# Performance work log

Hardware: AMD Instinct MI355X
Metric: run time of the kernel (lower is better)

## Reference

```python
import jax, jax.numpy as jnp
import numpy as np

N_NODES = 100000
N_EDGES = 1600000
F_IN, F_HID, F_OUT = 128, 128, 16
NEG_SLOPE = 0.2


def _glorot(key, shape):
    fan = sum(shape)
    return jax.random.uniform(key, shape, jnp.float32, -1.0, 1.0) * jnp.sqrt(6.0 / fan)


def setup_inputs() -> dict:
    key = jax.random.key(0)
    ks = jax.random.split(key, 16)
    x = jax.random.normal(ks[0], (N_NODES, F_IN), jnp.float32)
    edge_index = jax.random.randint(ks[1], (2, N_EDGES), 0, N_NODES, jnp.int64)
    d1, d2, d3 = F_HID, F_HID // 2, F_OUT
    return {
        'x': x,
        'edge_index': edge_index,
        'W1': _glorot(ks[2], (F_IN, d1)), 'a_src1': _glorot(ks[3], (d1,)), 'a_dst1': _glorot(ks[4], (d1,)), 'b1': jnp.zeros((d1,), jnp.float32),
        'W2': _glorot(ks[5], (d1, d2)), 'a_src2': _glorot(ks[6], (d2,)), 'a_dst2': _glorot(ks[7], (d2,)), 'b2': jnp.zeros((d2,), jnp.float32),
        'W3': _glorot(ks[8], (d2, d3)), 'a_src3': _glorot(ks[9], (d3,)), 'a_dst3': _glorot(ks[10], (d3,)), 'b3': jnp.zeros((d3,), jnp.float32),
    }


def gat_conv(x, src, dst, W, a_s, a_d, b):
    # x: [N, Fin] -> h: [N, Fout]; src/dst: [E] (self-loops included)
    h = x @ W
    e = jax.nn.leaky_relu(h @ a_s, NEG_SLOPE * 0 + NEG_SLOPE)  # placeholder avoided below
    # attention logits per edge: leaky_relu(alpha_src[src] + alpha_dst[dst])
    al_s = h @ a_s  # [N]
    al_d = h @ a_d  # [N]
    logits = jax.nn.leaky_relu(al_s[src] + al_d[dst], NEG_SLOPE)  # [E]
    # numerically stable softmax over incoming edges of each dst node
    m = jax.ops.segment_max(logits, dst, num_segments=N_NODES)
    m = jnp.where(jnp.isfinite(m), m, 0.0)
    ex = jnp.exp(logits - m[dst])
    denom = jax.ops.segment_sum(ex, dst, num_segments=N_NODES)
    alpha = ex / denom[dst]  # self-loops guarantee denom > 0
    out = jax.ops.segment_sum(alpha[:, None] * h[src], dst, num_segments=N_NODES)
    return out + b


def reference(x, edge_index, W1, a_src1, a_dst1, b1, W2, a_src2, a_dst2, b2, W3, a_src3, a_dst3, b3):
    loops = jnp.arange(N_NODES, dtype=edge_index.dtype)
    src = jnp.concatenate([edge_index[0], loops])
    dst = jnp.concatenate([edge_index[1], loops])
    h = gat_conv(x, src, dst, W1, a_src1, a_dst1, b1)
    h = jax.nn.relu(h)  # dropout p=0.5 is identity in eval mode
    h = gat_conv(h, src, dst, W2, a_src2, a_dst2, b2)
    h = jax.nn.relu(h)
    out = gat_conv(h, src, dst, W3, a_src3, a_dst3, b3)
    return out
```

## Files before the change

### kernel.cpp

```cpp
#include <hip/hip_runtime.h>
#include <hip/hip_bf16.h>

typedef __hip_bfloat16 bf16;
typedef __attribute__((ext_vector_type(8))) __bf16 bf16x8;
typedef __attribute__((ext_vector_type(4))) float f32x4;

static constexpr int N = 100000;
static constexpr int E = 1600000;
static constexpr int ETOT = E + N;
static constexpr float SLOPE = 0.2f;

__device__ __constant__ int c_poff[12] = {0, 16384, 16512, 16640,
                                          16768, 24960, 25024, 25088,
                                          25152, 26176, 26192, 26208};
static constexpr int PTOT = 26224;
static constexpr int H_POFF[12] = {0, 16384, 16512, 16640, 16768, 24960,
                                   25024, 25088, 25152, 26176, 26192, 26208};

struct Src12 { const void* p[12]; };

__device__ __forceinline__ float bfLo(unsigned u) { return __uint_as_float(u << 16); }
__device__ __forceinline__ float bfHi(unsigned u) { return __uint_as_float(u & 0xFFFF0000u); }

__device__ __forceinline__ void fma8(const uint4 r, float e, float* acc) {
  acc[0] = fmaf(e, bfLo(r.x), acc[0]);
  acc[1] = fmaf(e, bfHi(r.x), acc[1]);
  acc[2] = fmaf(e, bfLo(r.y), acc[2]);
  acc[3] = fmaf(e, bfHi(r.y), acc[3]);
  acc[4] = fmaf(e, bfLo(r.z), acc[4]);
  acc[5] = fmaf(e, bfHi(r.z), acc[5]);
  acc[6] = fmaf(e, bfLo(r.w), acc[6]);
  acc[7] = fmaf(e, bfHi(r.w), acc[7]);
}

__device__ __forceinline__ float edge_ex(float l) {
  l = (l > 0.f) ? l : SLOPE * l;
  return __expf(l);
}

__device__ __forceinline__ void loadEdge(const int* __restrict__ ei32,
                                         const long long* __restrict__ ei64,
                                         int use64, int t, int& s, int& d) {
  if (t >= E) { s = d = t - E; return; }
  if (use64) { s = (int)ei64[t]; d = (int)ei64[E + t]; }
  else       { s = ei32[t];      d = ei32[E + t]; }
}

__device__ __forceinline__ unsigned pk2(float a, float b) {
  bf16 x = __float2bfloat16(a), y = __float2bfloat16(b);
  unsigned short ux = *(unsigned short*)&x, uy = *(unsigned short*)&y;
  return ((unsigned)uy << 16) | ux;
}

static constexpr int CHUNK = 8192;
static constexpr int NCHK  = (ETOT + CHUNK - 1) / CHUNK;
static constexpr int NB1   = (N + 511) / 512;
static constexpr int M1    = NB1 * NCHK;
static constexpr int SBLK  = (M1 + 255) / 256;

__global__ __launch_bounds__(256) void detect_kernel(
    const unsigned long long* __restrict__ ei64,
    const unsigned short* __restrict__ w1u16, int* __restrict__ flags) {
  const int t = threadIdx.x;
  __shared__ unsigned long long bl[4];
  __shared__ unsigned long long sb64;
  const int w = t >> 6;
  bool p64 = (t < 64) && (ei64[t] >= (unsigned long long)N);
  unsigned long long b64 = __ballot(p64);
  if (t == 0) sb64 = b64;
  bool pf = (((w1u16[t] >> 7) & 0xFFu) >= 126u);
  unsigned long long bf_ = __ballot(pf);
  if ((t & 63) == 0) bl[w] = bf_;
  __syncthreads();
  if (t == 0) {
    flags[0] = (sb64 == 0ull) ? 1 : 0;
    flags[1] = ((bl[0] | bl[1] | bl[2] | bl[3]) != 0ull) ? 1 : 0;
  }
}

static constexpr int PB_PAR = (PTOT + 255) / 256;
static constexpr int PB_W1  = 128 * 128 / 256;
static constexpr int PB_W2  = 128 * 64 / 256;
static constexpr int PB_W3  = 64 * 16 / 256;
static constexpr int PB_TOT = NCHK + PB_PAR + PB_W1 + PB_W2 + PB_W3;

__device__ __forceinline__ void conv_w(const void* W, int kd, int dout, int f32,
                                       bf16* __restrict__ wt, int idx) {
  int n = idx / kd, k = idx - n * kd;
  float v = f32 ? ((const float*)W)[k * dout + n]
                : __bfloat162float(((const bf16*)W)[k * dout + n]);
  wt[idx] = __float2bfloat16(v);
}

__global__ __launch_bounds__(256) void prep_kernel(
    const int* __restrict__ ei32, const long long* __restrict__ ei64,
    const int* __restrict__ flags, int* __restrict__ c1,
    Src12 s, float* __restrict__ prm,
    bf16* __restrict__ w1t, bf16* __restrict__ w2t, bf16* __restrict__ w3t) {
  const int b = blockIdx.x, tid = threadIdx.x;
  const int f64 = flags[0], f32 = flags[1];
  if (b < NCHK) {
    __shared__ int h1[NB1];
    if (tid < NB1) h1[tid] = 0;
    __syncthreads();
    const int t0 = b * CHUNK;
#pragma unroll 4
    for (int i = tid; i < CHUNK; i += 256) {
      int t = t0 + i;
      if (t < ETOT) {
        int d = (t >= E) ? (t - E) : (f64 ? (int)ei64[E + t] : ei32[E + t]);
        atomicAdd(&h1[d >> 9], 1);
      }
    }
    __syncthreads();
    if (tid < NB1) c1[tid * NCHK + b] = h1[tid];
  } else if (b < NCHK + PB_PAR) {
    int t = (b - NCHK) * 256 + tid;
    if (t < PTOT) {
      int k = 0;
#pragma unroll
      for (int i = 1; i < 12; ++i)
        if (t >= c_poff[i]) k = i;
      int j = t - c_poff[k];
      prm[t] = f32 ? ((const float*)s.p[k])[j]
                   : __bfloat162float(((const bf16*)s.p[k])[j]);
    }
  } else if (b < NCHK + PB_PAR + PB_W1) {
    conv_w(s.p[0], 128, 128, f32, w1t, (b - NCHK - PB_PAR) * 256 + tid);
  } else if (b < NCHK + PB_PAR + PB_W1 + PB_W2) {
    conv_w(s.p[4], 128, 64, f32, w2t, (b - NCHK - PB_PAR - PB_W1) * 256 + tid);
  } else {
    conv_w(s.p[8], 64, 16, f32, w3t, (b - NCHK - PB_PAR - PB_W1 - PB_W2) * 256 + tid);
  }
}

__global__ __launch_bounds__(256) void scanA_kernel(const int* __restrict__ c1,
                                                    int* __restrict__ bsum) {
  __shared__ int red[256];
  const int t = threadIdx.x;
  const int i = blockIdx.x * 256 + t;
  red[t] = (i < M1) ? c1[i] : 0;
  __syncthreads();
#pragma unroll
  for (int off = 128; off > 0; off >>= 1) {
    if (t < off) red[t] += red[t + off];
    __syncthreads();
  }
  if (t == 0) bsum[blockIdx.x] = red[0];
}

__global__ __launch_bounds__(256) void scanB_kernel(const int* __restrict__ bsum,
                                                    int* __restrict__ boff) {
  __shared__ int s[256];
  const int t = threadIdx.x;
  const int v = (t < SBLK) ? bsum[t] : 0;
  s[t] = v;
  __syncthreads();
  for (int off = 1; off < 256; off <<= 1) {
    int u = (t >= off) ? s[t - off] : 0;
    __syncthreads();
    s[t] += u;
    __syncthreads();
  }
  if (t < SBLK) boff[t] = s[t] - v;
}

__global__ __launch_bounds__(256) void scanC_kernel(const int* __restrict__ c1,
                                                    const int* __restrict__ boff,
                                                    int* __restrict__ off1) {
  __shared__ int s[256];
  const int t = threadIdx.x;
  const int i = blockIdx.x * 256 + t;
  const int v = (i < M1) ? c1[i] : 0;
  s[t] = v;
  __syncthreads();
#pragma unroll
  for (int off = 1; off < 256; off <<= 1) {
    int u = (t >= off) ? s[t - off] : 0;
    __syncthreads();
    s[t] += u;
    __syncthreads();
  }
  if (i < M1) off1[i] = boff[blockIdx.x] + s[t] - v;
}

__device__ __forceinline__ void phaseC_body(int c, const int* __restrict__ ei32,
                                            const long long* __restrict__ ei64,
                                            int f64, const int* __restrict__ off1,
                                            int2* __restrict__ tmp) {
  __shared__ int cur[NB1];
  const int tid = threadIdx.x;
  if (tid < NB1) cur[tid] = off1[tid * NCHK + c];
  __syncthreads();
  const int t0 = c * CHUNK;
#pragma unroll 4
  for (int i = tid; i < CHUNK; i += 256) {
    int t = t0 + i;
    if (t < ETOT) {
      int s, d;
      loadEdge(ei32, ei64, f64, t, s, d);
      int pos = atomicAdd(&cur[d >> 9], 1);
      tmp[pos] = make_int2(d, s);
    }
  }
}

__global__ __launch_bounds__(256) void phaseD_kernel(const int* __restrict__ off1,
                                                     const int2* __restrict__ tmp,
                                                     int* __restrict__ rowptr,
                                                     int* __restrict__ ssrt) {
  __shared__ int h2[512], e2[512], cur[512];
  __shared__ int ps[256];
  const int b = blockIdx.x, t = threadIdx.x;
  const int base = off1[b * NCHK];
  const int end = (b + 1 < NB1) ? off1[(b + 1) * NCHK] : ETOT;
  const int len = end - base;
  h2[2 * t] = 0; h2[2 * t + 1] = 0;
  __syncthreads();
  for (int i = t; i < len; i += 256)
    atomicAdd(&h2[tmp[base + i].x & 511], 1);
  __syncthreads();
  const int s1 = h2[2 * t], s2 = h2[2 * t + 1];
  ps[t] = s1 + s2;
  __syncthreads();
  for (int off = 1; off < 256; off <<= 1) {
    int u = (t >= off) ? ps[t - off] : 0;
    __syncthreads();
    ps[t] += u;
    __syncthreads();
  }
  const int ep = ps[t] - (s1 + s2);
  e2[2 * t] = ep;
  e2[2 * t + 1] = ep + s1;
  cur[2 * t] = ep;
  cur[2 * t + 1] = ep + s1;
  __syncthreads();
#pragma unroll
  for (int k = 0; k < 2; ++k) {
    int f = 2 * t + k;
    int node = (b << 9) + f;
    if (node < N) rowptr[node] = base + e2[f];
  }
  if (b == 0 && t == 0) rowptr[N] = ETOT;
  for (int i = t; i < len; i += 256) {
    int2 e = tmp[base + i];
    int pos = base + atomicAdd(&cur[e.x & 511], 1);
    ssrt[pos] = e.y;
  }
}

template <int KD, int DOUT, bool XD>
__device__ __forceinline__ void gemm_body(int bb, const void* __restrict__ inv,
                                          const int* __restrict__ flags,
                                          const unsigned short* __restrict__ wt,
                                          bf16* __restrict__ h,
                                          const float* __restrict__ a_s,
                                          const float* __restrict__ a_d,
                                          float* __restrict__ als,
                                          float* __restrict__ ald) {
  constexpr int SA = KD + 8;
  constexpr int NT = DOUT / 16;
  constexpr int KS = KD / 32;
  __shared__ unsigned short sA[64 * SA];
  __shared__ unsigned short sB[DOUT * SA];
  const int tid = threadIdx.x;
  const int m0 = bb * 64;
  for (int idx = tid; idx < DOUT * KD / 8; idx += 256) {
    int n = idx / (KD / 8), k8 = idx - n * (KD / 8);
    *(uint4*)(sB + n * SA + k8 * 8) = *(const uint4*)(wt + n * KD + k8 * 8);
  }
  const bool f32 = XD ? (flags[1] != 0) : false;
  for (int idx = tid; idx < 64 * KD / 8; idx += 256) {
    int r = idx / (KD / 8), k8 = idx - r * (KD / 8);
    int m = m0 + r;
    uint4 v = make_uint4(0, 0, 0, 0);
    if (m < N) {
      if (XD && f32) {
        const float4 v0 = *((const float4*)inv + ((size_t)m * KD + k8 * 8) / 4);
        const float4 v1 = *((const float4*)inv + ((size_t)m * KD + k8 * 8) / 4 + 1);
        v = make_uint4(pk2(v0.x, v0.y), pk2(v0.z, v0.w),
                       pk2(v1.x, v1.y), pk2(v1.z, v1.w));
      } else {
        v = *((const uint4*)inv + ((size_t)m * KD + k8 * 8) / 8);
      }
    }
    *(uint4*)(sA + r * SA + k8 * 8) = v;
  }
  __syncthreads();
  const int lane = tid & 63;
  const int wv = tid >> 6;
  const int lr = lane & 15;
  const int q = lane >> 4;
  f32x4 acc[NT];
#pragma unroll
  for (int t = 0; t < NT; ++t)
#pragma unroll
    for (int r = 0; r < 4; ++r) acc[t][r] = 0.f;
  const int arow = wv * 16 + lr;
#pragma unroll
  for (int ks = 0; ks < KS; ++ks) {
    const int k0 = ks * 32 + q * 8;
    const bf16x8 a = *(const bf16x8*)(sA + arow * SA + k0);
#pragma unroll
    for (int t = 0; t < NT; ++t) {
      const bf16x8 b = *(const bf16x8*)(sB + (t * 16 + lr) * SA + k0);
      acc[t] = __builtin_amdgcn_mfma_f32_16x16x32_bf16(a, b, acc[t], 0, 0, 0);
    }
  }
  float ps[4] = {0.f, 0.f, 0.f, 0.f}, pd[4] = {0.f, 0.f, 0.f, 0.f};
#pragma unroll
  for (int t = 0; t < NT; ++t) {
    const float av = a_s[t * 16 + lr];
    const float dv = a_d[t * 16 + lr];
#pragma unroll
    for (int r = 0; r < 4; ++r) {
      ps[r] = fmaf(acc[t][r], av, ps[r]);
      pd[r] = fmaf(acc[t][r], dv, pd[r]);
    }
  }
#pragma unroll
  for (int m = 1; m < 16; m <<= 1)
#pragma unroll
    for (int r = 0; r < 4; ++r) {
      ps[r] += __shfl_xor(ps[r], m, 64);
      pd[r] += __shfl_xor(pd[r], m, 64);
    }
  const int mb = m0 + wv * 16 + q * 4;
  if (lr == 0) {
#pragma unroll
    for (int r = 0; r < 4; ++r) {
      int m = mb + r;
      if (m < N) { als[m] = ps[r]; ald[m] = pd[r]; }
    }
  }
#pragma unroll
  for (int t = 0; t < NT; ++t)
#pragma unroll
    for (int r = 0; r < 4; ++r) {
      int m = mb + r;
      if (m < N) h[(size_t)m * DOUT + t * 16 + lr] = __float2bfloat16(acc[t][r]);
    }
}

template <int KD, int DOUT>
__global__ __launch_bounds__(256) void gemm_al(const unsigned short* __restrict__ inb,
                                               const unsigned short* __restrict__ wt,
                                               bf16* __restrict__ h,
                                               const float* __restrict__ a_s,
                                               const float* __restrict__ a_d,
                                               float* __restrict__ als,
                                               float* __restrict__ ald) {
  gemm_body<KD, DOUT, false>(blockIdx.x, inb, nullptr, wt, h, a_s, a_d, als, ald);
}

static constexpr int GB1 = (N + 63) / 64;

__global__ __launch_bounds__(256) void gemm1_phaseC(
    const void* __restrict__ x, const int* __restrict__ flags,
    const unsigned short* __restrict__ wt, bf16* __restrict__ h,
    const float* __restrict__ a_s, const float* __restrict__ a_d,
    float* __restrict__ als, float* __restrict__ ald,
    const int* __restrict__ ei32, const long long* __restrict__ ei64,
    const int* __restrict__ off1, int2* __restrict__ tmp) {
  if (blockIdx.x < GB1) {
    gemm_body<128, 128, true>(blockIdx.x, x, flags, wt, h, a_s, a_d, als, ald);
  } else {
    int c = blockIdx.x - GB1;
    if (c < NCHK) phaseC_body(c, ei32, ei64, flags[0], off1, tmp);
  }
}

template <int DOUT, bool RELU, bool FINAL>
__global__ __launch_bounds__(256) void aggregate_csr(const int* __restrict__ rowptr,
                                                     const int* __restrict__ ssrt,
                                                     const float* __restrict__ als,
                                                     const float* __restrict__ ald,
                                                     const unsigned short* __restrict__ hb,
                                                     const float* __restrict__ bias,
                                                     bf16* __restrict__ outb,
                                                     void* __restrict__ outv,
                                                     const int* __restrict__ flags) {
  constexpr int TPN = DOUT / 8;
  constexpr int NPB = 256 / TPN;
  const int sub = threadIdx.x % TPN;
  const int d = blockIdx.x * NPB + threadIdx.x / TPN;
  if (d >= N) return;
  const int p0 = rowptr[d], p1 = rowptr[d + 1];
  const float ad = ald[d];
  const int col0 = sub * 8;
  float acc[8];
#pragma unroll
  for (int c = 0; c < 8; ++c) acc[c] = 0.f;
  float sum = 0.f;
  int p = p0;
  for (; p + 4 <= p1; p += 4) {
    const int s0 = ssrt[p + 0];
    const int s1 = ssrt[p + 1];
    const int s2 = ssrt[p + 2];
    const int s3 = ssrt[p + 3];
    const uint4 r0 = *reinterpret_cast<const uint4*>(hb + (size_t)s0 * DOUT + col0);
    const uint4 r1 = *reinterpret_cast<const uint4*>(hb + (size_t)s1 * DOUT + col0);
    const uint4 r2 = *reinterpret_cast<const uint4*>(hb + (size_t)s2 * DOUT + col0);
    const uint4 r3 = *reinterpret_cast<const uint4*>(hb + (size_t)s3 * DOUT + col0);
    const float x0 = edge_ex(als[s0] + ad);
    const float x1 = edge_ex(als[s1] + ad);
    const float x2 = edge_ex(als[s2] + ad);
    const float x3 = edge_ex(als[s3] + ad);
    sum += (x0 + x1) + (x2 + x3);
    fma8(r0, x0, acc);
    fma8(r1, x1, acc);
    fma8(r2, x2, acc);
    fma8(r3, x3, acc);
  }
  for (; p < p1; ++p) {
    const int s = ssrt[p];
    const uint4 r = *reinterpret_cast<const uint4*>(hb + (size_t)s * DOUT + col0);
    const float x = edge_ex(als[s] + ad);
    sum += x;
    fma8(r, x, acc);
  }
  const float inv = 1.f / sum;
  if (FINAL) {
    const bool f32o = flags[1] != 0;
#pragma unroll
    for (int c = 0; c < 8; ++c) {
      float v = acc[c] * inv + bias[col0 + c];
      if (f32o) ((float*)outv)[(size_t)d * DOUT + col0 + c] = v;
      else      ((bf16*)outv)[(size_t)d * DOUT + col0 + c] = __float2bfloat16(v);
    }
  } else {
#pragma unroll
    for (int c = 0; c < 8; ++c) {
      float v = acc[c] * inv + bias[col0 + c];
      if (RELU) v = (v > 0.f) ? v : 0.f;
      outb[(size_t)d * DOUT + col0 + c] = __float2bfloat16(v);
    }
  }
}

static inline size_t rup(size_t v) { return (v + 255) & ~(size_t)255; }

extern "C" void kernel_launch(void* const* d_in, const int* in_sizes, int n_in,
                              void* d_out, int out_size, void* d_ws, size_t ws_size,
                              hipStream_t stream) {
  const int* ei32 = (const int*)d_in[1];
  const long long* ei64 = (const long long*)d_in[1];

  char* p = (char*)d_ws;
  int*   flags  = (int*)p;   p += 256;
  float* prm    = (float*)p; p += rup((size_t)PTOT * 4);
  bf16*  w1t    = (bf16*)p;  p += rup((size_t)128 * 128 * 2);
  bf16*  w2t    = (bf16*)p;  p += rup((size_t)128 * 64 * 2);
  bf16*  w3t    = (bf16*)p;  p += rup((size_t)64 * 16 * 2);
  float* als    = (float*)p; p += rup((size_t)N * 4);
  float* ald    = (float*)p; p += rup((size_t)N * 4);
  int*   rowptr = (int*)p;   p += rup((size_t)(N + 1) * 4);
  int*   c1     = (int*)p;   p += rup((size_t)M1 * 4);
  int*   off1   = (int*)p;   p += rup((size_t)M1 * 4);
  int*   bsum   = (int*)p;   p += rup((size_t)SBLK * 4);
  int*   boff   = (int*)p;   p += rup((size_t)SBLK * 4);
  int2*  tmp    = (int2*)p;  p += rup((size_t)ETOT * 8);
  int*   ssrt   = (int*)p;   p += rup((size_t)ETOT * 4);
  bf16*  obuf   = (bf16*)p;  p += rup((size_t)N * 128 * 2);
  bf16*  hbuf   = (bf16*)p;

  Src12 s;
  for (int i = 0; i < 12; ++i) s.p[i] = d_in[2 + i];

  detect_kernel<<<1, 256, 0, stream>>>(
      (const unsigned long long*)d_in[1], (const unsigned short*)d_in[2], flags);
  prep_kernel<<<PB_TOT, 256, 0, stream>>>(ei32, ei64, flags, c1, s, prm, w1t, w2t, w3t);
  scanA_kernel<<<SBLK, 256, 0, stream>>>(c1, bsum);
  scanB_kernel<<<1, 256, 0, stream>>>(bsum, boff);
  scanC_kernel<<<SBLK, 256, 0, stream>>>(c1, boff, off1);

  const float *as1 = prm + H_POFF[1], *ad1 = prm + H_POFF[2], *b1 = prm + H_POFF[3];
  const float *as2 = prm + H_POFF[5], *ad2 = prm + H_POFF[6], *b2 = prm + H_POFF[7];
  const float *as3 = prm + H_POFF[9], *ad3 = prm + H_POFF[10], *b3 = prm + H_POFF[11];

  gemm1_phaseC<<<GB1 + NCHK, 256, 0, stream>>>(
      d_in[0], flags, (const unsigned short*)w1t, hbuf, as1, ad1, als, ald,
      ei32, ei64, off1, tmp);
  phaseD_kernel<<<NB1, 256, 0, stream>>>(off1, tmp, rowptr, ssrt);
  aggregate_csr<128, true, false><<<(N + 15) / 16, 256, 0, stream>>>(
      rowptr, ssrt, als, ald, (const unsigned short*)hbuf, b1, obuf, nullptr, flags);
  gemm_al<128, 64><<<GB1, 256, 0, stream>>>(
      (const unsigned short*)obuf, (const unsigned short*)w2t, hbuf, as2, ad2, als, ald);
  aggregate_csr<64, true, false><<<(N + 31) / 32, 256, 0, stream>>>(
      rowptr, ssrt, als, ald, (const unsigned short*)hbuf, b2, obuf, nullptr, flags);
  gemm_al<64, 16><<<GB1, 256, 0, stream>>>(
      (const unsigned short*)obuf, (const unsigned short*)w3t, hbuf, as3, ad3, als, ald);
  aggregate_csr<16, false, true><<<(N + 127) / 128, 256, 0, stream>>>(
      rowptr, ssrt, als, ald, (const unsigned short*)hbuf, b3, nullptr, d_out, flags);
}
```

Baseline: 332.6 us.

## Aggregate each destination node with a full wave splitting edges across lane groups

Replaces the per-node thread-group aggregation with one wavefront per destination node. Lanes are split into EPW edge slots by TPN feature lanes, with unrolled gathers and a shuffle-xor reduction at the end. The aim is more memory-level parallelism in the neighbour gathers for low-degree nodes (about 17 edges on average) and better latency hiding. In exchange, many lanes sit idle on the tail of each chunk, there is reduction overhead, and only one node is handled per wave, so blocks carry fewer nodes.

```diff
diff --git a/kernel.cpp b/kernel.cpp
--- a/kernel.cpp
+++ b/kernel.cpp
@@ -370,67 +370,83 @@
   }
 }
 
-template <int DOUT, bool RELU, bool FINAL>
-__global__ __launch_bounds__(256) void aggregate_csr(const int* __restrict__ rowptr,
-                                                     const int* __restrict__ ssrt,
-                                                     const float* __restrict__ als,
-                                                     const float* __restrict__ ald,
-                                                     const unsigned short* __restrict__ hb,
-                                                     const float* __restrict__ bias,
-                                                     bf16* __restrict__ outb,
-                                                     void* __restrict__ outv,
-                                                     const int* __restrict__ flags) {
-  constexpr int TPN = DOUT / 8;
-  constexpr int NPB = 256 / TPN;
-  const int sub = threadIdx.x % TPN;
-  const int d = blockIdx.x * NPB + threadIdx.x / TPN;
+template <int DOUT, int EPW, int U, bool RELU, bool FINAL>
+__global__ __launch_bounds__(256) void aggregate_wave(
+    const int* __restrict__ rowptr, const int* __restrict__ ssrt,
+    const float* __restrict__ als, const float* __restrict__ ald,
+    const unsigned short* __restrict__ hb, const float* __restrict__ bias,
+    bf16* __restrict__ outb, void* __restrict__ outv,
+    const int* __restrict__ flags) {
+  constexpr int TPN = 64 / EPW;
+  constexpr int V = DOUT / TPN;
+  static_assert(TPN * V == DOUT, "geometry");
+  const int wv = threadIdx.x >> 6;
+  const int lane = threadIdx.x & 63;
+  const int es = lane / TPN;
+  const int sub = lane % TPN;
+  const int d = blockIdx.x * 4 + wv;
   if (d >= N) return;
   const int p0 = rowptr[d], p1 = rowptr[d + 1];
   const float ad = ald[d];
-  const int col0 = sub * 8;
-  float acc[8];
-#pragma unroll
-  for (int c = 0; c < 8; ++c) acc[c] = 0.f;
+  const int col0 = sub * V;
+  float acc[V];
+#pragma unroll
+  for (int c = 0; c < V; ++c) acc[c] = 0.f;
   float sum = 0.f;
-  int p = p0;
-  for (; p + 4 <= p1; p += 4) {
-    const int s0 = ssrt[p + 0];
-    const int s1 = ssrt[p + 1];
-    const int s2 = ssrt[p + 2];
-    const int s3 = ssrt[p + 3];
-    const uint4 r0 = *reinterpret_cast<const uint4*>(hb + (size_t)s0 * DOUT + col0);
-    const uint4 r1 = *reinterpret_cast<const uint4*>(hb + (size_t)s1 * DOUT + col0);
-    const uint4 r2 = *reinterpret_cast<const uint4*>(hb + (size_t)s2 * DOUT + col0);
-    const uint4 r3 = *reinterpret_cast<const uint4*>(hb + (size_t)s3 * DOUT + col0);
-    const float x0 = edge_ex(als[s0] + ad);
-    const float x1 = edge_ex(als[s1] + ad);
-    const float x2 = edge_ex(als[s2] + ad);
-    const float x3 = edge_ex(als[s3] + ad);
-    sum += (x0 + x1) + (x2 + x3);
-    fma8(r0, x0, acc);
-    fma8(r1, x1, acc);
-    fma8(r2, x2, acc);
-    fma8(r3, x3, acc);
-  }
-  for (; p < p1; ++p) {
-    const int s = ssrt[p];
-    const uint4 r = *reinterpret_cast<const uint4*>(hb + (size_t)s * DOUT + col0);
-    const float x = edge_ex(als[s] + ad);
-    sum += x;
-    fma8(r, x, acc);
-  }
+  for (int base = p0; base < p1; base += EPW * U) {
+    int sv[U];
+    float xv[U];
+    uint4 r4[V == 8 ? U : 1];
+    uint2 r2[V == 4 ? U : 1];
+#pragma unroll
+    for (int u = 0; u < U; ++u) {
+      const int pp = base + es + u * EPW;
+      sv[u] = (pp < p1) ? ssrt[pp] : -1;
+    }
+#pragma unroll
+    for (int u = 0; u < U; ++u) {
+      xv[u] = 0.f;
+      if (sv[u] >= 0) {
+        const unsigned short* rp = hb + (size_t)sv[u] * DOUT + col0;
+        if constexpr (V == 8) r4[u] = *reinterpret_cast<const uint4*>(rp);
+        else                  r2[u] = *reinterpret_cast<const uint2*>(rp);
+        xv[u] = edge_ex(als[sv[u]] + ad);
+      }
+    }
+#pragma unroll
+    for (int u = 0; u < U; ++u) {
+      if (sv[u] >= 0) {
+        sum += xv[u];
+        if constexpr (V == 8) {
+          fma8(r4[u], xv[u], acc);
+        } else {
+          acc[0] = fmaf(xv[u], bfLo(r2[u].x), acc[0]);
+          acc[1] = fmaf(xv[u], bfHi(r2[u].x), acc[1]);
+          acc[2] = fmaf(xv[u], bfLo(r2[u].y), acc[2]);
+          acc[3] = fmaf(xv[u], bfHi(r2[u].y), acc[3]);
+        }
+      }
+    }
+  }
+#pragma unroll
+  for (int m = TPN; m < 64; m <<= 1) {
+#pragma unroll
+    for (int c = 0; c < V; ++c) acc[c] += __shfl_xor(acc[c], m, 64);
+    sum += __shfl_xor(sum, m, 64);
+  }
+  if (es != 0) return;
   const float inv = 1.f / sum;
   if (FINAL) {
     const bool f32o = flags[1] != 0;
 #pragma unroll
-    for (int c = 0; c < 8; ++c) {
+    for (int c = 0; c < V; ++c) {
       float v = acc[c] * inv + bias[col0 + c];
       if (f32o) ((float*)outv)[(size_t)d * DOUT + col0 + c] = v;
       else      ((bf16*)outv)[(size_t)d * DOUT + col0 + c] = __float2bfloat16(v);
     }
   } else {
 #pragma unroll
-    for (int c = 0; c < 8; ++c) {
+    for (int c = 0; c < V; ++c) {
       float v = acc[c] * inv + bias[col0 + c];
       if (RELU) v = (v > 0.f) ? v : 0.f;
       outb[(size_t)d * DOUT + col0 + c] = __float2bfloat16(v);
@@ -482,14 +498,14 @@
       d_in[0], flags, (const unsigned short*)w1t, hbuf, as1, ad1, als, ald,
       ei32, ei64, off1, tmp);
   phaseD_kernel<<<NB1, 256, 0, stream>>>(off1, tmp, rowptr, ssrt);
-  aggregate_csr<128, true, false><<<(N + 15) / 16, 256, 0, stream>>>(
+  aggregate_wave<128, 4, 5, true, false><<<(N + 3) / 4, 256, 0, stream>>>(
       rowptr, ssrt, als, ald, (const unsigned short*)hbuf, b1, obuf, nullptr, flags);
   gemm_al<128, 64><<<GB1, 256, 0, stream>>>(
       (const unsigned short*)obuf, (const unsigned short*)w2t, hbuf, as2, ad2, als, ald);
-  aggregate_csr<64, true, false><<<(N + 31) / 32, 256, 0, stream>>>(
+  aggregate_wave<64, 8, 3, true, false><<<(N + 3) / 4, 256, 0, stream>>>(
       rowptr, ssrt, als, ald, (const unsigned short*)hbuf, b2, obuf, nullptr, flags);
   gemm_al<64, 16><<<GB1, 256, 0, stream>>>(
       (const unsigned short*)obuf, (const unsigned short*)w3t, hbuf, as3, ad3, als, ald);
-  aggregate_csr<16, false, true><<<(N + 127) / 128, 256, 0, stream>>>(
+  aggregate_wave<16, 16, 2, false, true><<<(N + 3) / 4, 256, 0, stream>>>(
       rowptr, ssrt, als, ald, (const unsigned short*)hbuf, b3, nullptr, d_out, flags);
 }
```

New measurement: 353.0 us. 6.1% more time.

## Fuse layer aggregation with next-layer GEMM and attention projections

Applied to the files above, without the earlier changes.

Merges each hidden layer's CSR softmax aggregation (bias plus ReLU) with the following layer's MFMA GEMM and attention logit computation into one kernel. Aggregated rows go into shared memory instead of a global intermediate buffer. This removes two launches and the write and reread of the N×128 and N×64 intermediates. Separate als/ald and h buffers are used per layer so the fused kernels do not read and write the same arrays. The risk is lower occupancy from the larger LDS footprint, and a gather phase that now runs only 64 rows per block, which can reduce latency hiding.

```diff
diff --git a/kernel.cpp b/kernel.cpp
--- a/kernel.cpp
+++ b/kernel.cpp
@@ -342,17 +342,6 @@
     }
 }
 
-template <int KD, int DOUT>
-__global__ __launch_bounds__(256) void gemm_al(const unsigned short* __restrict__ inb,
-                                               const unsigned short* __restrict__ wt,
-                                               bf16* __restrict__ h,
-                                               const float* __restrict__ a_s,
-                                               const float* __restrict__ a_d,
-                                               float* __restrict__ als,
-                                               float* __restrict__ ald) {
-  gemm_body<KD, DOUT, false>(blockIdx.x, inb, nullptr, wt, h, a_s, a_d, als, ald);
-}
-
 static constexpr int GB1 = (N + 63) / 64;
 
 __global__ __launch_bounds__(256) void gemm1_phaseC(
@@ -368,6 +357,138 @@
     int c = blockIdx.x - GB1;
     if (c < NCHK) phaseC_body(c, ei32, ei64, flags[0], off1, tmp);
   }
+}
+
+template <int KD, int DOUT>
+__global__ __launch_bounds__(256) void agg_gemm(
+    const int* __restrict__ rowptr, const int* __restrict__ ssrt,
+    const float* __restrict__ als_in, const float* __restrict__ ald_in,
+    const unsigned short* __restrict__ hb, const float* __restrict__ bias_in,
+    const unsigned short* __restrict__ wt, bf16* __restrict__ hout,
+    const float* __restrict__ a_s, const float* __restrict__ a_d,
+    float* __restrict__ als_out, float* __restrict__ ald_out) {
+  constexpr int SA = KD + 8;
+  constexpr int NT = DOUT / 16;
+  constexpr int KS = KD / 32;
+  constexpr int TPN = KD / 8;
+  constexpr int NPB = 256 / TPN;
+  constexpr int NBAT = 64 / NPB;
+  __shared__ unsigned short sA[64 * SA];
+  __shared__ unsigned short sB[DOUT * SA];
+  const int tid = threadIdx.x;
+  const int m0 = blockIdx.x * 64;
+  for (int idx = tid; idx < DOUT * KD / 8; idx += 256) {
+    int n = idx / (KD / 8), k8 = idx - n * (KD / 8);
+    *(uint4*)(sB + n * SA + k8 * 8) = *(const uint4*)(wt + n * KD + k8 * 8);
+  }
+  const int sub = tid % TPN;
+  const int rb = tid / TPN;
+  const int col0 = sub * 8;
+#pragma unroll
+  for (int bat = 0; bat < NBAT; ++bat) {
+    const int r = bat * NPB + rb;
+    const int d = m0 + r;
+    uint4 w = make_uint4(0, 0, 0, 0);
+    if (d < N) {
+      const int p0 = rowptr[d], p1 = rowptr[d + 1];
+      const float ad = ald_in[d];
+      float acc[8];
+#pragma unroll
+      for (int c = 0; c < 8; ++c) acc[c] = 0.f;
+      float sum = 0.f;
+      int p = p0;
+      for (; p + 4 <= p1; p += 4) {
+        const int s0 = ssrt[p + 0];
+        const int s1 = ssrt[p + 1];
+        const int s2 = ssrt[p + 2];
+        const int s3 = ssrt[p + 3];
+        const uint4 r0 = *reinterpret_cast<const uint4*>(hb + (size_t)s0 * KD + col0);
+        const uint4 r1 = *reinterpret_cast<const uint4*>(hb + (size_t)s1 * KD + col0);
+        const uint4 r2 = *reinterpret_cast<const uint4*>(hb + (size_t)s2 * KD + col0);
+        const uint4 r3 = *reinterpret_cast<const uint4*>(hb + (size_t)s3 * KD + col0);
+        const float x0 = edge_ex(als_in[s0] + ad);
+        const float x1 = edge_ex(als_in[s1] + ad);
+        const float x2 = edge_ex(als_in[s2] + ad);
+        const float x3 = edge_ex(als_in[s3] + ad);
+        sum += (x0 + x1) + (x2 + x3);
+        fma8(r0, x0, acc);
+        fma8(r1, x1, acc);
+        fma8(r2, x2, acc);
+        fma8(r3, x3, acc);
+      }
+      for (; p < p1; ++p) {
+        const int s = ssrt[p];
+        const uint4 rr = *reinterpret_cast<const uint4*>(hb + (size_t)s * KD + col0);
+        const float x = edge_ex(als_in[s] + ad);
+        sum += x;
+        fma8(rr, x, acc);
+      }
+      const float inv = 1.f / sum;
+      float v[8];
+#pragma unroll
+      for (int c = 0; c < 8; ++c) {
+        float t = acc[c] * inv + bias_in[col0 + c];
+        v[c] = (t > 0.f) ? t : 0.f;
+      }
+      w = make_uint4(pk2(v[0], v[1]), pk2(v[2], v[3]),
+                     pk2(v[4], v[5]), pk2(v[6], v[7]));
+    }
+    *(uint4*)(sA + r * SA + col0) = w;
+  }
+  __syncthreads();
+  const int lane = tid & 63;
+  const int wv = tid >> 6;
+  const int lr = lane & 15;
+  const int q = lane >> 4;
+  f32x4 acc[NT];
+#pragma unroll
+  for (int t = 0; t < NT; ++t)
+#pragma unroll
+    for (int r = 0; r < 4; ++r) acc[t][r] = 0.f;
+  const int arow = wv * 16 + lr;
+#pragma unroll
+  for (int ks = 0; ks < KS; ++ks) {
+    const int k0 = ks * 32 + q * 8;
+    const bf16x8 a = *(const bf16x8*)(sA + arow * SA + k0);
+#pragma unroll
+    for (int t = 0; t < NT; ++t) {
+      const bf16x8 b = *(const bf16x8*)(sB + (t * 16 + lr) * SA + k0);
+      acc[t] = __builtin_amdgcn_mfma_f32_16x16x32_bf16(a, b, acc[t], 0, 0, 0);
+    }
+  }
+  float ps[4] = {0.f, 0.f, 0.f, 0.f}, pd[4] = {0.f, 0.f, 0.f, 0.f};
+#pragma unroll
+  for (int t = 0; t < NT; ++t) {
+    const float av = a_s[t * 16 + lr];
+    const float dv = a_d[t * 16 + lr];
+#pragma unroll
+    for (int r = 0; r < 4; ++r) {
+      ps[r] = fmaf(acc[t][r], av, ps[r]);
+      pd[r] = fmaf(acc[t][r], dv, pd[r]);
+    }
+  }
+#pragma unroll
+  for (int m = 1; m < 16; m <<= 1)
+#pragma unroll
+    for (int r = 0; r < 4; ++r) {
+      ps[r] += __shfl_xor(ps[r], m, 64);
+      pd[r] += __shfl_xor(pd[r], m, 64);
+    }
+  const int mb = m0 + wv * 16 + q * 4;
+  if (lr == 0) {
+#pragma unroll
+    for (int r = 0; r < 4; ++r) {
+      int m = mb + r;
+      if (m < N) { als_out[m] = ps[r]; ald_out[m] = pd[r]; }
+    }
+  }
+#pragma unroll
+  for (int t = 0; t < NT; ++t)
+#pragma unroll
+    for (int r = 0; r < 4; ++r) {
+      int m = mb + r;
+      if (m < N) hout[(size_t)m * DOUT + t * 16 + lr] = __float2bfloat16(acc[t][r]);
+    }
 }
 
 template <int DOUT, bool RELU, bool FINAL>
@@ -452,8 +573,10 @@
   bf16*  w1t    = (bf16*)p;  p += rup((size_t)128 * 128 * 2);
   bf16*  w2t    = (bf16*)p;  p += rup((size_t)128 * 64 * 2);
   bf16*  w3t    = (bf16*)p;  p += rup((size_t)64 * 16 * 2);
-  float* als    = (float*)p; p += rup((size_t)N * 4);
-  float* ald    = (float*)p; p += rup((size_t)N * 4);
+  float* als1   = (float*)p; p += rup((size_t)N * 4);
+  float* ald1   = (float*)p; p += rup((size_t)N * 4);
+  float* als2   = (float*)p; p += rup((size_t)N * 4);
+  float* ald2   = (float*)p; p += rup((size_t)N * 4);
   int*   rowptr = (int*)p;   p += rup((size_t)(N + 1) * 4);
   int*   c1     = (int*)p;   p += rup((size_t)M1 * 4);
   int*   off1   = (int*)p;   p += rup((size_t)M1 * 4);
@@ -461,8 +584,9 @@
   int*   boff   = (int*)p;   p += rup((size_t)SBLK * 4);
   int2*  tmp    = (int2*)p;  p += rup((size_t)ETOT * 8);
   int*   ssrt   = (int*)p;   p += rup((size_t)ETOT * 4);
-  bf16*  obuf   = (bf16*)p;  p += rup((size_t)N * 128 * 2);
-  bf16*  hbuf   = (bf16*)p;
+  bf16*  h1     = (bf16*)p;  p += rup((size_t)N * 128 * 2);
+  bf16*  h2     = (bf16*)p;  p += rup((size_t)N * 64 * 2);
+  bf16*  h3     = (bf16*)p;
 
   Src12 s;
   for (int i = 0; i < 12; ++i) s.p[i] = d_in[2 + i];
@@ -479,17 +603,15 @@
   const float *as3 = prm + H_POFF[9], *ad3 = prm + H_POFF[10], *b3 = prm + H_POFF[11];
 
   gemm1_phaseC<<<GB1 + NCHK, 256, 0, stream>>>(
-      d_in[0], flags, (const unsigned short*)w1t, hbuf, as1, ad1, als, ald,
+      d_in[0], flags, (const unsigned short*)w1t, h1, as1, ad1, als1, ald1,
       ei32, ei64, off1, tmp);
   phaseD_kernel<<<NB1, 256, 0, stream>>>(off1, tmp, rowptr, ssrt);
-  aggregate_csr<128, true, false><<<(N + 15) / 16, 256, 0, stream>>>(
-      rowptr, ssrt, als, ald, (const unsigned short*)hbuf, b1, obuf, nullptr, flags);
-  gemm_al<128, 64><<<GB1, 256, 0, stream>>>(
-      (const unsigned short*)obuf, (const unsigned short*)w2t, hbuf, as2, ad2, als, ald);
-  aggregate_csr<64, true, false><<<(N + 31) / 32, 256, 0, stream>>>(
-      rowptr, ssrt, als, ald, (const unsigned short*)hbuf, b2, obuf, nullptr, flags);
-  gemm_al<64, 16><<<GB1, 256, 0, stream>>>(
-      (const unsigned short*)obuf, (const unsigned short*)w3t, hbuf, as3, ad3, als, ald);
+  agg_gemm<128, 64><<<GB1, 256, 0, stream>>>(
+      rowptr, ssrt, als1, ald1, (const unsigned short*)h1, b1,
+      (const unsigned short*)w2t, h2, as2, ad2, als2, ald2);
+  agg_gemm<64, 16><<<GB1, 256, 0, stream>>>(
+      rowptr, ssrt, als2, ald2, (const unsigned short*)h2, b2,
+      (const unsigned short*)w3t, h3, as3, ad3, als1, ald1);
   aggregate_csr<16, false, true><<<(N + 127) / 128, 256, 0, stream>>>(
-      rowptr, ssrt, als, ald, (const unsigned short*)hbuf, b3, nullptr, d_out, flags);
-}
+      rowptr, ssrt, als1, ald1, (const unsigned short*)h3, b3, nullptr, d_out, flags);
+}
```

New measurement: 329.7 us. Within noise of the previous version (-0.9%).

## Store hidden features in 16-column slabs and aggregate per slab for locality

Applied to the files above, without the earlier changes.

Feature matrices move from row-major [N, D] to slab-major layout [D/16][N][16], written by the GEMM epilogue and read by the next GEMM. A new agg_slab kernel assigns each block to one slab, so each block's random gathers touch a 3.2 MB slab instead of full 256-byte rows, aiming for better L2/MALL hit rates. The cost is that the per-node alpha logits are recomputed redundantly once per slab. The final 16-wide aggregation now uses 4-wide vectors so more threads work on each node, and als/ald buffers are double-buffered so consecutive layers do not overwrite each other. The tmp buffer is reused as storage for the second-layer output.

```diff
diff --git a/kernel.cpp b/kernel.cpp
--- a/kernel.cpp
+++ b/kernel.cpp
@@ -31,6 +31,13 @@
   acc[5] = fmaf(e, bfHi(r.z), acc[5]);
   acc[6] = fmaf(e, bfLo(r.w), acc[6]);
   acc[7] = fmaf(e, bfHi(r.w), acc[7]);
+}
+
+__device__ __forceinline__ void fma4(const uint2 r, float e, float* acc) {
+  acc[0] = fmaf(e, bfLo(r.x), acc[0]);
+  acc[1] = fmaf(e, bfHi(r.x), acc[1]);
+  acc[2] = fmaf(e, bfLo(r.y), acc[2]);
+  acc[3] = fmaf(e, bfHi(r.y), acc[3]);
 }
 
 __device__ __forceinline__ float edge_ex(float l) {
@@ -249,7 +256,7 @@
   }
 }
 
-template <int KD, int DOUT, bool XD>
+template <int KD, int DOUT, bool XD, int ASLAB>
 __device__ __forceinline__ void gemm_body(int bb, const void* __restrict__ inv,
                                           const int* __restrict__ flags,
                                           const unsigned short* __restrict__ wt,
@@ -280,6 +287,9 @@
         const float4 v1 = *((const float4*)inv + ((size_t)m * KD + k8 * 8) / 4 + 1);
         v = make_uint4(pk2(v0.x, v0.y), pk2(v0.z, v0.w),
                        pk2(v1.x, v1.y), pk2(v1.z, v1.w));
+      } else if (ASLAB > 0) {
+        const unsigned short* inS = (const unsigned short*)inv;
+        v = *(const uint4*)(inS + ((size_t)(k8 >> 1) * N + m) * 16 + (k8 & 1) * 8);
       } else {
         v = *((const uint4*)inv + ((size_t)m * KD + k8 * 8) / 8);
       }
@@ -338,19 +348,8 @@
 #pragma unroll
     for (int r = 0; r < 4; ++r) {
       int m = mb + r;
-      if (m < N) h[(size_t)m * DOUT + t * 16 + lr] = __float2bfloat16(acc[t][r]);
-    }
-}
-
-template <int KD, int DOUT>
-__global__ __launch_bounds__(256) void gemm_al(const unsigned short* __restrict__ inb,
-                                               const unsigned short* __restrict__ wt,
-                                               bf16* __restrict__ h,
-                                               const float* __restrict__ a_s,
-                                               const float* __restrict__ a_d,
-                                               float* __restrict__ als,
-                                               float* __restrict__ ald) {
-  gemm_body<KD, DOUT, false>(blockIdx.x, inb, nullptr, wt, h, a_s, a_d, als, ald);
+      if (m < N) h[((size_t)t * N + m) * 16 + lr] = __float2bfloat16(acc[t][r]);
+    }
 }
 
 static constexpr int GB1 = (N + 63) / 64;
@@ -363,11 +362,80 @@
     const int* __restrict__ ei32, const long long* __restrict__ ei64,
     const int* __restrict__ off1, int2* __restrict__ tmp) {
   if (blockIdx.x < GB1) {
-    gemm_body<128, 128, true>(blockIdx.x, x, flags, wt, h, a_s, a_d, als, ald);
+    gemm_body<128, 128, true, 0>(blockIdx.x, x, flags, wt, h, a_s, a_d, als, ald);
   } else {
     int c = blockIdx.x - GB1;
     if (c < NCHK) phaseC_body(c, ei32, ei64, flags[0], off1, tmp);
   }
+}
+
+template <int KD, int DOUT, int ASLAB>
+__global__ __launch_bounds__(256) void gemm_al(const unsigned short* __restrict__ inb,
+                                               const unsigned short* __restrict__ wt,
+                                               bf16* __restrict__ h,
+                                               const float* __restrict__ a_s,
+                                               const float* __restrict__ a_d,
+                                               float* __restrict__ als,
+                                               float* __restrict__ ald) {
+  gemm_body<KD, DOUT, false, ASLAB>(blockIdx.x, inb, nullptr, wt, h, a_s, a_d, als, ald);
+}
+
+template <int NSLAB>
+__global__ __launch_bounds__(256) void agg_slab(
+    const int* __restrict__ rowptr, const int* __restrict__ ssrt,
+    const float* __restrict__ als, const float* __restrict__ ald,
+    const unsigned short* __restrict__ hbS, const float* __restrict__ bias,
+    unsigned short* __restrict__ hAs) {
+  const int slab = blockIdx.x % NSLAB;
+  const int d = (blockIdx.x / NSLAB) * 128 + (threadIdx.x >> 1);
+  if (d >= N) return;
+  const int sub = threadIdx.x & 1;
+  const int co = sub * 8;
+  const size_t sbase = (size_t)slab * N;
+  const unsigned short* hs = hbS + sbase * 16 + co;
+  const int p0 = rowptr[d], p1 = rowptr[d + 1];
+  const float ad = ald[d];
+  float acc[8];
+#pragma unroll
+  for (int c = 0; c < 8; ++c) acc[c] = 0.f;
+  float sum = 0.f;
+  int p = p0;
+  for (; p + 4 <= p1; p += 4) {
+    const int s0 = __builtin_nontemporal_load(ssrt + p + 0);
+    const int s1 = __builtin_nontemporal_load(ssrt + p + 1);
+    const int s2 = __builtin_nontemporal_load(ssrt + p + 2);
+    const int s3 = __builtin_nontemporal_load(ssrt + p + 3);
+    const uint4 r0 = *reinterpret_cast<const uint4*>(hs + (size_t)s0 * 16);
+    const uint4 r1 = *reinterpret_cast<const uint4*>(hs + (size_t)s1 * 16);
+    const uint4 r2 = *reinterpret_cast<const uint4*>(hs + (size_t)s2 * 16);
+    const uint4 r3 = *reinterpret_cast<const uint4*>(hs + (size_t)s3 * 16);
+    const float x0 = edge_ex(als[s0] + ad);
+    const float x1 = edge_ex(als[s1] + ad);
+    const float x2 = edge_ex(als[s2] + ad);
+    const float x3 = edge_ex(als[s3] + ad);
+    sum += (x0 + x1) + (x2 + x3);
+    fma8(r0, x0, acc);
+    fma8(r1, x1, acc);
+    fma8(r2, x2, acc);
+    fma8(r3, x3, acc);
+  }
+  for (; p < p1; ++p) {
+    const int s = __builtin_nontemporal_load(ssrt + p);
+    const uint4 rr = *reinterpret_cast<const uint4*>(hs + (size_t)s * 16);
+    const float x = edge_ex(als[s] + ad);
+    sum += x;
+    fma8(rr, x, acc);
+  }
+  const float inv = 1.f / sum;
+  float v[8];
+#pragma unroll
+  for (int c = 0; c < 8; ++c) {
+    float t = acc[c] * inv + bias[slab * 16 + co + c];
+    v[c] = (t > 0.f) ? t : 0.f;
+  }
+  const uint4 w = make_uint4(pk2(v[0], v[1]), pk2(v[2], v[3]),
+                             pk2(v[4], v[5]), pk2(v[6], v[7]));
+  *(uint4*)(hAs + (sbase + d) * 16 + co) = w;
 }
 
 template <int DOUT, bool RELU, bool FINAL>
@@ -380,17 +448,18 @@
                                                      bf16* __restrict__ outb,
                                                      void* __restrict__ outv,
                                                      const int* __restrict__ flags) {
-  constexpr int TPN = DOUT / 8;
+  constexpr int V = (DOUT >= 64) ? 8 : 4;
+  constexpr int TPN = DOUT / V;
   constexpr int NPB = 256 / TPN;
   const int sub = threadIdx.x % TPN;
   const int d = blockIdx.x * NPB + threadIdx.x / TPN;
   if (d >= N) return;
   const int p0 = rowptr[d], p1 = rowptr[d + 1];
   const float ad = ald[d];
-  const int col0 = sub * 8;
-  float acc[8];
-#pragma unroll
-  for (int c = 0; c < 8; ++c) acc[c] = 0.f;
+  const int col0 = sub * V;
+  float acc[V];
+#pragma unroll
+  for (int c = 0; c < V; ++c) acc[c] = 0.f;
   float sum = 0.f;
   int p = p0;
   for (; p + 4 <= p1; p += 4) {
@@ -398,39 +467,55 @@
     const int s1 = ssrt[p + 1];
     const int s2 = ssrt[p + 2];
     const int s3 = ssrt[p + 3];
-    const uint4 r0 = *reinterpret_cast<const uint4*>(hb + (size_t)s0 * DOUT + col0);
-    const uint4 r1 = *reinterpret_cast<const uint4*>(hb + (size_t)s1 * DOUT + col0);
-    const uint4 r2 = *reinterpret_cast<const uint4*>(hb + (size_t)s2 * DOUT + col0);
-    const uint4 r3 = *reinterpret_cast<const uint4*>(hb + (size_t)s3 * DOUT + col0);
     const float x0 = edge_ex(als[s0] + ad);
     const float x1 = edge_ex(als[s1] + ad);
     const float x2 = edge_ex(als[s2] + ad);
     const float x3 = edge_ex(als[s3] + ad);
     sum += (x0 + x1) + (x2 + x3);
-    fma8(r0, x0, acc);
-    fma8(r1, x1, acc);
-    fma8(r2, x2, acc);
-    fma8(r3, x3, acc);
+    if constexpr (V == 8) {
+      const uint4 r0 = *reinterpret_cast<const uint4*>(hb + (size_t)s0 * DOUT + col0);
+      const uint4 r1 = *reinterpret_cast<const uint4*>(hb + (size_t)s1 * DOUT + col0);
+      const uint4 r2 = *reinterpret_cast<const uint4*>(hb + (size_t)s2 * DOUT + col0);
+      const uint4 r3 = *reinterpret_cast<const uint4*>(hb + (size_t)s3 * DOUT + col0);
+      fma8(r0, x0, acc);
+      fma8(r1, x1, acc);
+      fma8(r2, x2, acc);
+      fma8(r3, x3, acc);
+    } else {
+      const uint2 r0 = *reinterpret_cast<const uint2*>(hb + (size_t)s0 * DOUT + col0);
+      const uint2 r1 = *reinterpret_cast<const uint2*>(hb + (size_t)s1 * DOUT + col0);
+      const uint2 r2 = *reinterpret_cast<const uint2*>(hb + (size_t)s2 * DOUT + col0);
+      const uint2 r3 = *reinterpret_cast<const uint2*>(hb + (size_t)s3 * DOUT + col0);
+      fma4(r0, x0, acc);
+      fma4(r1, x1, acc);
+      fma4(r2, x2, acc);
+      fma4(r3, x3, acc);
+    }
   }
   for (; p < p1; ++p) {
     const int s = ssrt[p];
-    const uint4 r = *reinterpret_cast<const uint4*>(hb + (size_t)s * DOUT + col0);
     const float x = edge_ex(als[s] + ad);
     sum += x;
-    fma8(r, x, acc);
+    if constexpr (V == 8) {
+      const uint4 r = *reinterpret_cast<const uint4*>(hb + (size_t)s * DOUT + col0);
+      fma8(r, x, acc);
+    } else {
+      const uint2 r = *reinterpret_cast<const uint2*>(hb + (size_t)s * DOUT + col0);
+      fma4(r, x, acc);
+    }
   }
   const float inv = 1.f / sum;
   if (FINAL) {
     const bool f32o = flags[1] != 0;
 #pragma unroll
-    for (int c = 0; c < 8; ++c) {
+    for (int c = 0; c < V; ++c) {
       float v = acc[c] * inv + bias[col0 + c];
       if (f32o) ((float*)outv)[(size_t)d * DOUT + col0 + c] = v;
       else      ((bf16*)outv)[(size_t)d * DOUT + col0 + c] = __float2bfloat16(v);
     }
   } else {
 #pragma unroll
-    for (int c = 0; c < 8; ++c) {
+    for (int c = 0; c < V; ++c) {
       float v = acc[c] * inv + bias[col0 + c];
       if (RELU) v = (v > 0.f) ? v : 0.f;
       outb[(size_t)d * DOUT + col0 + c] = __float2bfloat16(v);
@@ -452,8 +537,10 @@
   bf16*  w1t    = (bf16*)p;  p += rup((size_t)128 * 128 * 2);
   bf16*  w2t    = (bf16*)p;  p += rup((size_t)128 * 64 * 2);
   bf16*  w3t    = (bf16*)p;  p += rup((size_t)64 * 16 * 2);
-  float* als    = (float*)p; p += rup((size_t)N * 4);
-  float* ald    = (float*)p; p += rup((size_t)N * 4);
+  float* als1   = (float*)p; p += rup((size_t)N * 4);
+  float* ald1   = (float*)p; p += rup((size_t)N * 4);
+  float* als2   = (float*)p; p += rup((size_t)N * 4);
+  float* ald2   = (float*)p; p += rup((size_t)N * 4);
   int*   rowptr = (int*)p;   p += rup((size_t)(N + 1) * 4);
   int*   c1     = (int*)p;   p += rup((size_t)M1 * 4);
   int*   off1   = (int*)p;   p += rup((size_t)M1 * 4);
@@ -461,8 +548,11 @@
   int*   boff   = (int*)p;   p += rup((size_t)SBLK * 4);
   int2*  tmp    = (int2*)p;  p += rup((size_t)ETOT * 8);
   int*   ssrt   = (int*)p;   p += rup((size_t)ETOT * 4);
-  bf16*  obuf   = (bf16*)p;  p += rup((size_t)N * 128 * 2);
-  bf16*  hbuf   = (bf16*)p;
+  bf16*  h1s    = (bf16*)p;  p += rup((size_t)8 * N * 16 * 2);
+  bf16*  hA1s   = (bf16*)p;  p += rup((size_t)8 * N * 16 * 2);
+  bf16*  h2s    = (bf16*)p;  p += rup((size_t)4 * N * 16 * 2);
+  bf16*  h3     = (bf16*)p;  p += rup((size_t)N * 16 * 2);
+  bf16*  hA2s   = (bf16*)tmp;
 
   Src12 s;
   for (int i = 0; i < 12; ++i) s.p[i] = d_in[2 + i];
@@ -479,17 +569,21 @@
   const float *as3 = prm + H_POFF[9], *ad3 = prm + H_POFF[10], *b3 = prm + H_POFF[11];
 
   gemm1_phaseC<<<GB1 + NCHK, 256, 0, stream>>>(
-      d_in[0], flags, (const unsigned short*)w1t, hbuf, as1, ad1, als, ald,
+      d_in[0], flags, (const unsigned short*)w1t, h1s, as1, ad1, als1, ald1,
       ei32, ei64, off1, tmp);
   phaseD_kernel<<<NB1, 256, 0, stream>>>(off1, tmp, rowptr, ssrt);
-  aggregate_csr<128, true, false><<<(N + 15) / 16, 256, 0, stream>>>(
-      rowptr, ssrt, als, ald, (const unsigned short*)hbuf, b1, obuf, nullptr, flags);
-  gemm_al<128, 64><<<GB1, 256, 0, stream>>>(
-      (const unsigned short*)obuf, (const unsigned short*)w2t, hbuf, as2, ad2, als, ald);
-  aggregate_csr<64, true, false><<<(N + 31) / 32, 256, 0, stream>>>(
-      rowptr, ssrt, als, ald, (const unsigned short*)hbuf, b2, obuf, nullptr, flags);
-  gemm_al<64, 16><<<GB1, 256, 0, stream>>>(
-      (const unsigned short*)obuf, (const unsigned short*)w3t, hbuf, as3, ad3, als, ald);
-  aggregate_csr<16, false, true><<<(N + 127) / 128, 256, 0, stream>>>(
-      rowptr, ssrt, als, ald, (const unsigned short*)hbuf, b3, nullptr, d_out, flags);
-}
+  agg_slab<8><<<((N + 127) / 128) * 8, 256, 0, stream>>>(
+      rowptr, ssrt, als1, ald1, (const unsigned short*)h1s, b1,
+      (unsigned short*)hA1s);
+  gemm_al<128, 64, 8><<<GB1, 256, 0, stream>>>(
+      (const unsigned short*)hA1s, (const unsigned short*)w2t, h2s,
+      as2, ad2, als2, ald2);
+  agg_slab<4><<<((N + 127) / 128) * 4, 256, 0, stream>>>(
+      rowptr, ssrt, als2, ald2, (const unsigned short*)h2s, b2,
+      (unsigned short*)hA2s);
+  gemm_al<64, 16, 4><<<GB1, 256, 0, stream>>>(
+      (const unsigned short*)hA2s, (const unsigned short*)w3t, h3,
+      as3, ad3, als1, ald1);
+  aggregate_csr<16, false, true><<<(N + 63) / 64, 256, 0, stream>>>(
+      rowptr, ssrt, als1, ald1, (const unsigned short*)h3, b3, nullptr, d_out, flags);
+}
```

Result: slower. 534.2 us (+60.6%).
